# Kernel optimization log

Measured on AMD Instinct MI355X. Metric: run time of the kernel, lower is better.

## Reference

```python
import jax, jax.numpy as jnp
import numpy as np

B, DIM, SIZE = 16, 512, 128

def _conv2d(x, w, pad_h, pad_w):
    # x: [B,C,H,W], w: [O,I,kh,kw]
    return jax.lax.conv_general_dilated(
        x, w, window_strides=(1, 1),
        padding=((pad_h, pad_h), (pad_w, pad_w)),
        dimension_numbers=('NCHW', 'OIHW', 'NCHW'))


def setup_inputs() -> dict:
    key = jax.random.key(0)
    ks = jax.random.split(key, 8)
    s = SIZE
    return {
        'x': jax.random.normal(ks[0], (B, DIM, s, s), dtype=jnp.float32),
        'w_conv': jax.random.normal(ks[1], (2, DIM, 1, 1), dtype=jnp.float32) * (1.0 / np.sqrt(DIM)),
        'w_ww_conv': jax.random.normal(ks[2], (1, 2, s, 5), dtype=jnp.float32) * (1.0 / np.sqrt(2 * s * 5)),
        'w_hw_conv': jax.random.normal(ks[3], (1, 2, 5, s), dtype=jnp.float32) * (1.0 / np.sqrt(2 * s * 5)),
        'ww_lin_w': jax.random.normal(ks[4], (s, s), dtype=jnp.float32) * (1.0 / np.sqrt(s)),
        'ww_lin_b': jax.random.normal(ks[5], (s,), dtype=jnp.float32) * 0.01,
        'hw_lin_w': jax.random.normal(ks[6], (s, s), dtype=jnp.float32) * (1.0 / np.sqrt(s)),
        'hw_lin_b': jax.random.normal(ks[7], (s,), dtype=jnp.float32) * 0.01,
    }


def reference(x, w_conv, w_ww_conv, w_hw_conv, ww_lin_w, ww_lin_b, hw_lin_w, hw_lin_b):
    # 1x1 conv dim -> 2 (no bias, no bn, no act): pure channel GEMM
    x2 = jnp.einsum('bchw,oc->bohw', x, w_conv[:, :, 0, 0])  # [B,2,S,S]

    # ww branch: conv kernel (SIZE,5), pad (0,2) -> [B,1,1,S]
    ww = _conv2d(x2, w_ww_conv, 0, 2)[:, 0, 0, :]            # [B,S]
    ww = jax.nn.sigmoid(ww @ ww_lin_w.T + ww_lin_b)          # Linear + Sigmoid

    # hw branch: conv kernel (5,SIZE), pad (2,0) -> [B,1,S,1]
    hw = _conv2d(x2, w_hw_conv, 2, 0)[:, 0, :, 0]            # [B,S]
    hw = jax.nn.sigmoid(hw @ hw_lin_w.T + hw_lin_b)

    # batched outer product hw (S,1) @ ww (1,S) -> [B,S,S]
    return jnp.einsum('bh,bw->bhw', hw, ww)
```

## Files before the change

kernel.cpp:

```cpp
#include <hip/hip_runtime.h>
#include <math.h>

#define BB   16
#define CC   512
#define SS   128
#define HWSZ (SS * SS)

__global__ __launch_bounds__(256) void k1_channel_reduce(
    const float* __restrict__ x, const float* __restrict__ wconv,
    float* __restrict__ x2, float* __restrict__ x2t)
{
    __shared__ float wsA[CC];
    __shared__ float wsB[CC];
    __shared__ float red[2][8][SS];

    const int tid = threadIdx.x;
    for (int i = tid; i < CC; i += 256) {
        wsA[i] = wconv[i];
        wsB[i] = wconv[CC + i];
    }
    __syncthreads();

    const int bh = blockIdx.x;
    const int b  = bh >> 7;
    const int h  = bh & 127;
    const int wl = tid & 31;
    const int cg = tid >> 5;
    const size_t base = (size_t)b * CC * HWSZ + (size_t)h * SS + (size_t)(wl * 4);

    float4 a0 = make_float4(0.f, 0.f, 0.f, 0.f);
    float4 a1 = make_float4(0.f, 0.f, 0.f, 0.f);
    #pragma unroll 4
    for (int c = cg; c < CC; c += 8) {
        const float4 xv = *(const float4*)(x + base + (size_t)c * HWSZ);
        const float wa = wsA[c];
        const float wb = wsB[c];
        a0.x = fmaf(xv.x, wa, a0.x); a0.y = fmaf(xv.y, wa, a0.y);
        a0.z = fmaf(xv.z, wa, a0.z); a0.w = fmaf(xv.w, wa, a0.w);
        a1.x = fmaf(xv.x, wb, a1.x); a1.y = fmaf(xv.y, wb, a1.y);
        a1.z = fmaf(xv.z, wb, a1.z); a1.w = fmaf(xv.w, wb, a1.w);
    }
    *(float4*)&red[0][cg][wl * 4] = a0;
    *(float4*)&red[1][cg][wl * 4] = a1;
    __syncthreads();

    const int o = tid >> 7;
    const int w = tid & 127;
    float s = 0.f;
    #pragma unroll
    for (int g = 0; g < 8; ++g) s += red[o][g][w];
    x2 [((size_t)(b * 2 + o) * SS + h) * SS + w] = s;
    x2t[((size_t)(b * 2 + o) * SS + w) * SS + h] = s;
}

__global__ __launch_bounds__(256) void k2_rest(
    const float* __restrict__ x2, const float* __restrict__ x2t,
    const float* __restrict__ wwc,
    const float* __restrict__ hwc,
    const float* __restrict__ wlw, const float* __restrict__ wlb,
    const float* __restrict__ hlw, const float* __restrict__ hlb,
    float* __restrict__ out)
{
    __shared__ float tw[2][5][SS];
    __shared__ float uh[2][5][SS];
    __shared__ float vbuf[2 * SS];
    __shared__ float rbuf[2 * SS];

    const int b        = blockIdx.x;
    const int tid      = threadIdx.x;
    const int lane_pos = tid & 127;
    const int half     = tid >> 7;
    const int half_u   = __builtin_amdgcn_readfirstlane(half);

    {
        const float* xrow = x2 + (size_t)(b * 2 + half) * HWSZ + lane_pos;
        const float* wrow = wwc + half_u * (SS * 5);
        float acc[5] = {0.f, 0.f, 0.f, 0.f, 0.f};
        for (int kh = 0; kh < SS; ++kh) {
            const float xv = xrow[(size_t)kh * SS];
            #pragma unroll
            for (int kw = 0; kw < 5; ++kw)
                acc[kw] = fmaf(xv, wrow[kh * 5 + kw], acc[kw]);
        }
        #pragma unroll
        for (int kw = 0; kw < 5; ++kw) tw[half][kw][lane_pos] = acc[kw];
    }

    {
        const float* xcol = x2t + (size_t)(b * 2 + half) * HWSZ + lane_pos;
        const float* wrow = hwc + half_u * (5 * SS);
        float acc[5] = {0.f, 0.f, 0.f, 0.f, 0.f};
        for (int kw = 0; kw < SS; ++kw) {
            const float xv = xcol[(size_t)kw * SS];
            #pragma unroll
            for (int kh = 0; kh < 5; ++kh)
                acc[kh] = fmaf(xv, wrow[kh * SS + kw], acc[kh]);
        }
        #pragma unroll
        for (int kh = 0; kh < 5; ++kh) uh[half][kh][lane_pos] = acc[kh];
    }
    __syncthreads();

    {
        float s = 0.f;
        if (half == 0) {
            const int wo = lane_pos;
            #pragma unroll
            for (int kw = 0; kw < 5; ++kw) {
                const int wsrc = wo + kw - 2;
                if (wsrc >= 0 && wsrc < SS) s += tw[0][kw][wsrc] + tw[1][kw][wsrc];
            }
        } else {
            const int ho = lane_pos;
            #pragma unroll
            for (int kh = 0; kh < 5; ++kh) {
                const int hsrc = ho + kh - 2;
                if (hsrc >= 0 && hsrc < SS) s += uh[0][kh][hsrc] + uh[1][kh][hsrc];
            }
        }
        vbuf[tid] = s;
    }
    __syncthreads();

    {
        const int j = lane_pos;
        const float* lw  = (half == 0) ? wlw : hlw;
        const float* lb  = (half == 0) ? wlb : hlb;
        const float* vin = vbuf + half * SS;
        float s = lb[j];
        const float4* wr = (const float4*)(lw + (size_t)j * SS);
        #pragma unroll 4
        for (int k4 = 0; k4 < SS / 4; ++k4) {
            const float4 wv = wr[k4];
            s = fmaf(vin[4 * k4 + 0], wv.x, s);
            s = fmaf(vin[4 * k4 + 1], wv.y, s);
            s = fmaf(vin[4 * k4 + 2], wv.z, s);
            s = fmaf(vin[4 * k4 + 3], wv.w, s);
        }
        rbuf[tid] = 1.f / (1.f + expf(-s));
    }
    __syncthreads();

    {
        float* ob = out + (size_t)b * HWSZ;
        for (int p4 = tid; p4 < HWSZ / 4; p4 += 256) {
            const int h  = p4 >> 5;
            const int w0 = (p4 & 31) * 4;
            const float hv = rbuf[SS + h];
            float4 o;
            o.x = hv * rbuf[w0 + 0];
            o.y = hv * rbuf[w0 + 1];
            o.z = hv * rbuf[w0 + 2];
            o.w = hv * rbuf[w0 + 3];
            *(float4*)(ob + (size_t)h * SS + w0) = o;
        }
    }
}

extern "C" void kernel_launch(void* const* d_in, const int* in_sizes, int n_in,
                              void* d_out, int out_size, void* d_ws, size_t ws_size,
                              hipStream_t stream) {
    const float* x     = (const float*)d_in[0];
    const float* wconv = (const float*)d_in[1];
    const float* wwc   = (const float*)d_in[2];
    const float* hwc   = (const float*)d_in[3];
    const float* wlw   = (const float*)d_in[4];
    const float* wlb   = (const float*)d_in[5];
    const float* hlw   = (const float*)d_in[6];
    const float* hlb   = (const float*)d_in[7];
    float* out = (float*)d_out;

    float* x2  = (float*)d_ws;
    float* x2t = x2 + (size_t)BB * 2 * HWSZ;

    k1_channel_reduce<<<dim3(BB * SS), dim3(256), 0, stream>>>(x, wconv, x2, x2t);
    k2_rest<<<dim3(BB), dim3(256), 0, stream>>>(x2, x2t, wwc, hwc,
                                                wlw, wlb, hlw, hlb, out);
}
```

Measured before the change: 710.7 us.

## Give each k1 thread the full channel loop, dropping the shared-memory reduction

Restructures the channel-reduction kernel so each 128-thread block handles four rows and each thread accumulates over all channels itself. This removes the shared-memory cross-group reduction and its barrier, and makes the x2 stores float4. It reduces the block count and per-thread parallelism over channels, which risks poor latency hiding on a memory-bound load stream. The x2t stores also become strided scalar writes. It adds unroll pragmas to the k2 convolution loops.

```diff
diff --git a/kernel.cpp b/kernel.cpp
--- a/kernel.cpp
+++ b/kernel.cpp
@@ -6,51 +6,52 @@
 #define SS   128
 #define HWSZ (SS * SS)
 
-__global__ __launch_bounds__(256) void k1_channel_reduce(
+__global__ __launch_bounds__(128) void k1_channel_reduce(
     const float* __restrict__ x, const float* __restrict__ wconv,
     float* __restrict__ x2, float* __restrict__ x2t)
 {
     __shared__ float wsA[CC];
     __shared__ float wsB[CC];
-    __shared__ float red[2][8][SS];
 
     const int tid = threadIdx.x;
-    for (int i = tid; i < CC; i += 256) {
+    for (int i = tid; i < CC; i += 128) {
         wsA[i] = wconv[i];
         wsB[i] = wconv[CC + i];
     }
     __syncthreads();
 
-    const int bh = blockIdx.x;
-    const int b  = bh >> 7;
-    const int h  = bh & 127;
-    const int wl = tid & 31;
-    const int cg = tid >> 5;
-    const size_t base = (size_t)b * CC * HWSZ + (size_t)h * SS + (size_t)(wl * 4);
+    const int b  = blockIdx.x >> 5;
+    const int tg = blockIdx.x & 31;
+    const float* xp = x + (size_t)b * CC * HWSZ + (size_t)tg * (4 * SS) + tid * 4;
 
     float4 a0 = make_float4(0.f, 0.f, 0.f, 0.f);
     float4 a1 = make_float4(0.f, 0.f, 0.f, 0.f);
-    #pragma unroll 4
-    for (int c = cg; c < CC; c += 8) {
-        const float4 xv = *(const float4*)(x + base + (size_t)c * HWSZ);
+    #pragma unroll 8
+    for (int c = 0; c < CC; ++c) {
+        const float4 v = *(const float4*)(xp + (size_t)c * HWSZ);
         const float wa = wsA[c];
         const float wb = wsB[c];
-        a0.x = fmaf(xv.x, wa, a0.x); a0.y = fmaf(xv.y, wa, a0.y);
-        a0.z = fmaf(xv.z, wa, a0.z); a0.w = fmaf(xv.w, wa, a0.w);
-        a1.x = fmaf(xv.x, wb, a1.x); a1.y = fmaf(xv.y, wb, a1.y);
-        a1.z = fmaf(xv.z, wb, a1.z); a1.w = fmaf(xv.w, wb, a1.w);
+        a0.x = fmaf(v.x, wa, a0.x); a0.y = fmaf(v.y, wa, a0.y);
+        a0.z = fmaf(v.z, wa, a0.z); a0.w = fmaf(v.w, wa, a0.w);
+        a1.x = fmaf(v.x, wb, a1.x); a1.y = fmaf(v.y, wb, a1.y);
+        a1.z = fmaf(v.z, wb, a1.z); a1.w = fmaf(v.w, wb, a1.w);
     }
-    *(float4*)&red[0][cg][wl * 4] = a0;
-    *(float4*)&red[1][cg][wl * 4] = a1;
-    __syncthreads();
 
-    const int o = tid >> 7;
-    const int w = tid & 127;
-    float s = 0.f;
-    #pragma unroll
-    for (int g = 0; g < 8; ++g) s += red[o][g][w];
-    x2 [((size_t)(b * 2 + o) * SS + h) * SS + w] = s;
-    x2t[((size_t)(b * 2 + o) * SS + w) * SS + h] = s;
+    const int hloc = tid >> 5;
+    const int w0   = (tid & 31) * 4;
+    const int h    = tg * 4 + hloc;
+
+    *(float4*)&x2[((size_t)(b * 2 + 0) * SS + h) * SS + w0] = a0;
+    *(float4*)&x2[((size_t)(b * 2 + 1) * SS + h) * SS + w0] = a1;
+
+    x2t[((size_t)(b * 2 + 0) * SS + (w0 + 0)) * SS + h] = a0.x;
+    x2t[((size_t)(b * 2 + 0) * SS + (w0 + 1)) * SS + h] = a0.y;
+    x2t[((size_t)(b * 2 + 0) * SS + (w0 + 2)) * SS + h] = a0.z;
+    x2t[((size_t)(b * 2 + 0) * SS + (w0 + 3)) * SS + h] = a0.w;
+    x2t[((size_t)(b * 2 + 1) * SS + (w0 + 0)) * SS + h] = a1.x;
+    x2t[((size_t)(b * 2 + 1) * SS + (w0 + 1)) * SS + h] = a1.y;
+    x2t[((size_t)(b * 2 + 1) * SS + (w0 + 2)) * SS + h] = a1.z;
+    x2t[((size_t)(b * 2 + 1) * SS + (w0 + 3)) * SS + h] = a1.w;
 }
 
 __global__ __launch_bounds__(256) void k2_rest(
@@ -76,6 +77,7 @@
         const float* xrow = x2 + (size_t)(b * 2 + half) * HWSZ + lane_pos;
         const float* wrow = wwc + half_u * (SS * 5);
         float acc[5] = {0.f, 0.f, 0.f, 0.f, 0.f};
+        #pragma unroll 8
         for (int kh = 0; kh < SS; ++kh) {
             const float xv = xrow[(size_t)kh * SS];
             #pragma unroll
@@ -90,6 +92,7 @@
         const float* xcol = x2t + (size_t)(b * 2 + half) * HWSZ + lane_pos;
         const float* wrow = hwc + half_u * (5 * SS);
         float acc[5] = {0.f, 0.f, 0.f, 0.f, 0.f};
+        #pragma unroll 8
         for (int kw = 0; kw < SS; ++kw) {
             const float xv = xcol[(size_t)kw * SS];
             #pragma unroll
@@ -173,7 +176,7 @@
     float* x2  = (float*)d_ws;
     float* x2t = x2 + (size_t)BB * 2 * HWSZ;
 
-    k1_channel_reduce<<<dim3(BB * SS), dim3(256), 0, stream>>>(x, wconv, x2, x2t);
+    k1_channel_reduce<<<dim3(BB * 32), dim3(128), 0, stream>>>(x, wconv, x2, x2t);
     k2_rest<<<dim3(BB), dim3(256), 0, stream>>>(x2, x2t, wwc, hwc,
                                                 wlw, wlb, hlw, hlb, out);
 }
```

After: 693.2 us. -2.5%, faster.
